# Performance work log

Hardware: AMD Instinct MI355X
Metric: run time of the kernel (lower is better)

## Reference

```python
import jax, jax.numpy as jnp
import numpy as np

NEG_SLOPE = 0.2  # PyG GATConv default negative_slope
N_NODES = 50000


def gat_conv(x, src, dst, W, att_src, att_dst, bias, heads, out_ch):
    # x: [N, F_in]; src/dst: [E] (messages flow src -> dst, softmax over dst)
    N = x.shape[0]
    h = (x @ W).reshape(N, heads, out_ch)              # [N,H,C]
    a_src = jnp.sum(h * att_src, axis=-1)              # [N,H]
    a_dst = jnp.sum(h * att_dst, axis=-1)              # [N,H]
    e = jax.nn.leaky_relu(a_src[src] + a_dst[dst], NEG_SLOPE)   # [E,H]
    # numerically stable segment softmax over incoming edges of each dst node
    m = jax.ops.segment_max(e, dst, num_segments=N)    # [N,H]
    e = jnp.exp(e - m[dst])
    denom = jax.ops.segment_sum(e, dst, num_segments=N)
    alpha = e / (denom[dst] + 1e-16)                   # [E,H]
    msg = h[src] * alpha[:, :, None]                   # [E,H,C]
    out = jax.ops.segment_sum(msg, dst, num_segments=N)  # [N,H,C]
    return out.reshape(N, heads * out_ch) + bias


def add_self_loops(edge_index, num_nodes):
    loop = jnp.arange(num_nodes, dtype=edge_index.dtype)
    return jnp.concatenate([edge_index, jnp.stack([loop, loop])], axis=1)


def setup_inputs() -> dict:
    key = jax.random.key(0)
    ks = jax.random.split(key, 10)
    F_in, H, C, F_out = 256, 4, 64, 16
    x = jax.random.normal(ks[0], (N_NODES, F_in), dtype=jnp.float32)
    edge_index = jax.random.randint(ks[1], (2, 800000), 0, N_NODES, dtype=jnp.int64)
    s1 = 1.0 / np.sqrt(F_in)
    s2 = 1.0 / np.sqrt(H * C)
    return {
        "x": x,
        "edge_index": edge_index,
        "W1": jax.random.normal(ks[2], (F_in, H * C), dtype=jnp.float32) * s1,
        "att_src1": jax.random.normal(ks[3], (H, C), dtype=jnp.float32) * s2,
        "att_dst1": jax.random.normal(ks[4], (H, C), dtype=jnp.float32) * s2,
        "b1": jnp.zeros((H * C,), dtype=jnp.float32),
        "W2": jax.random.normal(ks[5], (H * C, F_out), dtype=jnp.float32) * s2,
        "att_src2": jax.random.normal(ks[6], (1, F_out), dtype=jnp.float32) * 0.25,
        "att_dst2": jax.random.normal(ks[7], (1, F_out), dtype=jnp.float32) * 0.25,
        "b2": jnp.zeros((F_out,), dtype=jnp.float32),
    }


def reference(x, edge_index, W1, att_src1, att_dst1, b1, W2, att_src2, att_dst2, b2):
    ei = add_self_loops(edge_index, x.shape[0])
    src, dst = ei[0], ei[1]
    H1, C1 = att_src1.shape
    h = gat_conv(x, src, dst, W1, att_src1, att_dst1, b1, H1, C1)
    h = jax.nn.relu(h)
    # F.dropout(training=False) is identity in eval mode
    H2, C2 = att_src2.shape
    out = gat_conv(h, src, dst, W2, att_src2, att_dst2, b2, H2, C2)
    return jax.nn.log_softmax(out, axis=1)
```

## Files before the change

### kernel.cpp

```cpp
#include <hip/hip_runtime.h>
#include <math.h>


typedef __attribute__((ext_vector_type(8))) short bf16x8;
typedef __attribute__((ext_vector_type(8))) unsigned short u16x8;
typedef __attribute__((ext_vector_type(4))) float f32x4;
typedef __attribute__((ext_vector_type(2))) float f32x2;

#define BCAP 1536

static __device__ inline unsigned short f2bf(float f) {
    unsigned u = __builtin_bit_cast(unsigned, f);
    unsigned r = (u + 0x7FFF + ((u >> 16) & 1)) >> 16;
    return (unsigned short)r;
}
static __device__ inline float bf2f(unsigned short u) {
    unsigned v = ((unsigned)u) << 16;
    return __builtin_bit_cast(float, v);
}
static __device__ inline float lrelu(float x) { return x > 0.f ? x : 0.2f * x; }

__global__ __launch_bounds__(256) void k_prep(const float* __restrict__ x,
                                              const float* __restrict__ W1,
                                              const float* __restrict__ b1,
                                              const float* __restrict__ W2,
                                              short* __restrict__ xb,
                                              unsigned short* __restrict__ csr,
                                              short* __restrict__ w1t,
                                              float* __restrict__ b1p,
                                              float* __restrict__ w2p,
                                              int* __restrict__ fill_bkt,
                                              float* __restrict__ a1s,
                                              float* __restrict__ a2s,
                                              unsigned* __restrict__ h1f8u,
                                              float* __restrict__ h2,
                                              int N, int nbuk) {
    long idx = (long)blockIdx.x * 256 + threadIdx.x;
    const long T = (long)N * 32;
    if (idx < T) {
        const float* xp = x + idx * 8;
        float4 f0 = *(const float4*)xp;
        float4 f1 = *(const float4*)(xp + 4);
        short b[8];
        b[0] = (short)f2bf(f0.x); b[1] = (short)f2bf(f0.y);
        b[2] = (short)f2bf(f0.z); b[3] = (short)f2bf(f0.w);
        b[4] = (short)f2bf(f1.x); b[5] = (short)f2bf(f1.y);
        b[6] = (short)f2bf(f1.z); b[7] = (short)f2bf(f1.w);
        *(bf16x8*)(xb + idx * 8) = *(bf16x8*)&b[0];
    }
    if (idx < (long)N * 16) {
        ushort4 v = make_ushort4((unsigned short)N, (unsigned short)N,
                                 (unsigned short)N, (unsigned short)N);
        if ((idx & 15) == 0) v.x = (unsigned short)(idx >> 4);
        *(ushort4*)(csr + idx * 4) = v;
    }
    if (idx < nbuk) fill_bkt[idx] = 0;
    if (idx < 256) {
        int ct = ((int)idx >> 6) * 64 + ((int)idx & 3) * 16 + (((int)idx & 63) >> 2);
        b1p[idx] = b1[ct];
    }
    if (idx < 4096) {
        int pp = (int)idx >> 4, c2 = (int)idx & 15;
        int ct = (pp >> 6) * 64 + (pp & 3) * 16 + ((pp & 63) >> 2);
        w2p[idx] = W2[ct * 16 + c2];
    }
    if (idx < 4) a1s[(long)N * 4 + idx] = -1e30f;
    if (idx == 4) a2s[N] = -1e30f;
    if (idx < 64) h1f8u[(long)N * 64 + idx] = 0u;
    if (idx < 16) h2[(long)N * 16 + idx] = 0.f;
    if (idx < 65536) {
        int n = (int)idx >> 8, k = (int)idx & 255;
        w1t[n * 256 + k] = (short)f2bf(W1[k * 256 + n]);
    }
}

__global__ __launch_bounds__(256) void k_bucketize(const int* __restrict__ ei,
                                                   int* __restrict__ fill_bkt,
                                                   unsigned* __restrict__ tmp,
                                                   int E0, int nbuk) {
    __shared__ int hist[1024];
    __shared__ int base[1024];
    const int t = threadIdx.x;
    const int e0 = blockIdx.x * 4096;
    for (int b = t; b < nbuk; b += 256) hist[b] = 0;
    __syncthreads();
    int ss[16], ds[16];
    int nm = 0;
#pragma unroll
    for (int k = 0; k < 16; ++k) {
        int e = e0 + t + k * 256;
        if (e < E0) {
            ss[nm] = ei[e];
            ds[nm] = ei[E0 + e];
            atomicAdd(&hist[ds[nm] >> 6], 1);
            ++nm;
        }
    }
    __syncthreads();
    for (int b = t; b < nbuk; b += 256) {
        int c = hist[b];
        base[b] = c ? atomicAdd(&fill_bkt[b], c) : 0;
        hist[b] = 0;
    }
    __syncthreads();
    for (int k = 0; k < nm; ++k) {
        int b = ds[k] >> 6;
        int r = base[b] + atomicAdd(&hist[b], 1);
        if (r < BCAP)
            tmp[(long)b * BCAP + r] = (unsigned)ss[k] | ((unsigned)(ds[k] & 63) << 16);
    }
}

__global__ __launch_bounds__(256) void k_gemm1_fill(
        const short* __restrict__ Ab,
        const short* __restrict__ Bt,
        const float* __restrict__ att_s,
        const float* __restrict__ att_d,
        unsigned char* __restrict__ C8,
        float* __restrict__ a1s,
        float* __restrict__ a1d,
        int M,
        const unsigned* __restrict__ tmp,
        const int* __restrict__ fill_bkt,
        int* __restrict__ cnt,
        unsigned short* __restrict__ csr,
        int N, int nbuk) {
    __shared__ short As[64][40];
    __shared__ short Bs[128][40];
    __shared__ int lfill[64];

    if ((int)blockIdx.x < nbuk) {
        const int b = blockIdx.x;
        const int t = threadIdx.x;
        if (t < 64) lfill[t] = 0;
        __syncthreads();
        int c = min(fill_bkt[b], BCAP);
        const unsigned* tp = tmp + (long)b * BCAP;
        for (int i = t; i < c; i += 256) {
            unsigned u = tp[i];
            int dl = u >> 16;
            int slot = atomicAdd(&lfill[dl], 1);
            if (slot < 63)
                csr[(((long)b * 64 + dl) << 6) + 1 + slot] = (unsigned short)(u & 0xffff);
        }
        __syncthreads();
        if (t < 64) {
            int d = b * 64 + t;
            if (d < N) cnt[d] = 1 + min(lfill[t], 63);
        }
        return;
    }

    const int g = (int)blockIdx.x - nbuk;
    const int bm = (g >> 1) * 64;
    const int bn = (g & 1) * 128;
    const int tid = threadIdx.x;
    const int lane = tid & 63;
    const int wave = tid >> 6;
    const int wm = (wave >> 1) * 32;
    const int wn = (wave & 1) * 64;
    const int l15 = lane & 15;
    const int l4 = lane >> 4;

    const int ar = tid >> 2, aq = (tid & 3) * 8;
    const int br = tid >> 1, bh = (tid & 1) * 16;

    f32x4 acc[2][4] = {};

    for (int k0 = 0; k0 < 256; k0 += 32) {
        {
            bf16x8 av;
            if (bm + ar < M) {
                av = *(const bf16x8*)&Ab[(long)(bm + ar) * 256 + k0 + aq];
            } else {
#pragma unroll
                for (int q = 0; q < 8; ++q) av[q] = 0;
            }
            *(bf16x8*)&As[ar][aq] = av;
            const short* p = &Bt[(long)(bn + br) * 256 + k0 + bh];
            *(bf16x8*)&Bs[br][bh] = *(const bf16x8*)p;
            *(bf16x8*)&Bs[br][bh + 8] = *(const bf16x8*)(p + 8);
        }
        __syncthreads();

        bf16x8 af[2], bfr[4];
#pragma unroll
        for (int i = 0; i < 2; ++i)
            af[i] = *(const bf16x8*)&As[wm + i * 16 + l15][l4 * 8];
#pragma unroll
        for (int j = 0; j < 4; ++j)
            bfr[j] = *(const bf16x8*)&Bs[wn + j * 16 + l15][l4 * 8];
#pragma unroll
        for (int i = 0; i < 2; ++i)
#pragma unroll
            for (int j = 0; j < 4; ++j)
                acc[i][j] = __builtin_amdgcn_mfma_f32_16x16x32_bf16(af[i], bfr[j], acc[i][j], 0, 0, 0);
        __syncthreads();
    }

    const int h = (bn + wn) >> 6;
    float aws[4], awd[4];
#pragma unroll
    for (int j = 0; j < 4; ++j) {
        aws[j] = att_s[h * 64 + j * 16 + l15];
        awd[j] = att_d[h * 64 + j * 16 + l15];
    }

#pragma unroll
    for (int i = 0; i < 2; ++i) {
#pragma unroll
        for (int r = 0; r < 4; ++r) {
            float sv = 0.f, dv = 0.f;
#pragma unroll
            for (int j = 0; j < 4; ++j) {
                sv += acc[i][j][r] * aws[j];
                dv += acc[i][j][r] * awd[j];
            }
#pragma unroll
            for (int o = 1; o < 16; o <<= 1) {
                sv += __shfl_xor(sv, o);
                dv += __shfl_xor(dv, o);
            }
            int row = bm + wm + i * 16 + l4 * 4 + r;
            if (row < M) {
                if (l15 == 0) { a1s[row * 4 + h] = sv; a1d[row * 4 + h] = dv; }
                int d = 0;
                d = __builtin_amdgcn_cvt_pk_fp8_f32(acc[i][0][r], acc[i][1][r], d, false);
                d = __builtin_amdgcn_cvt_pk_fp8_f32(acc[i][2][r], acc[i][3][r], d, true);
                *(unsigned*)&C8[(long)row * 256 + (bn + wn) + l15 * 4] = (unsigned)d;
            }
        }
    }
}

__global__ __launch_bounds__(256) void k_gather1(const unsigned char* __restrict__ h1f8,
                                                 const int* __restrict__ cnt,
                                                 const unsigned short* __restrict__ csr,
                                                 const float* __restrict__ as1,
                                                 const float* __restrict__ ad1,
                                                 const float* __restrict__ b1p,
                                                 unsigned short* __restrict__ out1b,
                                                 int N) {
    int wid = blockIdx.x * 4 + (threadIdx.x >> 6);
    int lane = threadIdx.x & 63;
    if (wid >= N) return;

    const int es = lane >> 4;
    const int cl = lane & 15;
    const int hc = cl >> 2;
    const float adh = ad1[wid * 4 + hc];

    int c = min(cnt[wid], 64);
    int len4 = (c + 3) & ~3;
    const unsigned short* seg = csr + ((long)wid << 6);
    const char* as1c = (const char*)as1 + hc * 4;
    const char* h1c  = (const char*)h1f8 + cl * 16;

    float dacc = 0.f;
    f32x2 acc2[8] = {};
#pragma unroll 2
    for (int j0 = 0; j0 < len4; j0 += 4) {
        int sv = seg[j0 + es];
        float a = __expf(lrelu(*(const float*)(as1c + ((long)sv << 4)) + adh));
        dacc += a;
        f32x2 av = {a, a};
        uint4 v = *(const uint4*)(h1c + ((long)sv << 8));
        unsigned w[4] = {v.x, v.y, v.z, v.w};
#pragma unroll
        for (int q = 0; q < 4; ++q) {
            f32x2 lo = __builtin_amdgcn_cvt_pk_f32_fp8((int)w[q], false);
            f32x2 hi = __builtin_amdgcn_cvt_pk_f32_fp8((int)w[q], true);
            acc2[q * 2 + 0] += av * lo;
            acc2[q * 2 + 1] += av * hi;
        }
    }
    dacc += __shfl_xor(dacc, 16);
    dacc += __shfl_xor(dacc, 32);
    const float inv_c = 1.f / (dacc + 1e-16f);

    float accf[16];
#pragma unroll
    for (int q = 0; q < 8; ++q) { accf[2 * q] = acc2[q].x; accf[2 * q + 1] = acc2[q].y; }
#pragma unroll
    for (int q = 0; q < 16; ++q) {
        accf[q] += __shfl_xor(accf[q], 16);
        accf[q] += __shfl_xor(accf[q], 32);
    }
    if (lane < 16) {
        unsigned pk[8];
#pragma unroll
        for (int q = 0; q < 8; ++q) {
            float v0 = fmaxf(accf[q * 2 + 0] * inv_c + b1p[cl * 16 + q * 2 + 0], 0.f);
            float v1 = fmaxf(accf[q * 2 + 1] * inv_c + b1p[cl * 16 + q * 2 + 1], 0.f);
            pk[q] = (unsigned)f2bf(v0) | ((unsigned)f2bf(v1) << 16);
        }
        unsigned short* dst = &out1b[(long)wid * 256 + cl * 16];
        *(uint4*)dst = make_uint4(pk[0], pk[1], pk[2], pk[3]);
        *(uint4*)(dst + 8) = make_uint4(pk[4], pk[5], pk[6], pk[7]);
    }
}

__global__ __launch_bounds__(256) void k_gemm2(const unsigned short* __restrict__ Xb,
                                               const float* __restrict__ Wp,
                                               const float* __restrict__ att_s,
                                               const float* __restrict__ att_d,
                                               float* __restrict__ h2,
                                               float* __restrict__ a2s,
                                               float* __restrict__ a2d, int N) {
    __shared__ float Ws[256 * 16];
    for (int i = threadIdx.x; i < 1024; i += 256)
        ((float4*)Ws)[i] = ((const float4*)Wp)[i];
    __syncthreads();
    int r = threadIdx.x >> 4, c = threadIdx.x & 15;
    int row = blockIdx.x * 16 + r;
    if (row >= N) return;
    const unsigned short* xr = Xb + (long)row * 256;
    float acc = 0.f;
    for (int k = 0; k < 256; k += 8) {
        u16x8 xv = *(const u16x8*)&xr[k];
#pragma unroll
        for (int q = 0; q < 8; ++q)
            acc += bf2f(xv[q]) * Ws[(k + q) * 16 + c];
    }
    h2[row * 16 + c] = acc;
    float vs = acc * att_s[c];
    float vd = acc * att_d[c];
    for (int o = 1; o < 16; o <<= 1) { vs += __shfl_xor(vs, o); vd += __shfl_xor(vd, o); }
    if (c == 0) { a2s[row] = vs; a2d[row] = vd; }
}

__global__ __launch_bounds__(256) void k_gather2(const float* __restrict__ h2,
                                                 const int* __restrict__ cnt,
                                                 const unsigned short* __restrict__ csr,
                                                 const float* __restrict__ a2s,
                                                 const float* __restrict__ a2d,
                                                 const float* __restrict__ b2,
                                                 float* __restrict__ out, int N) {
    int wid = blockIdx.x * 4 + (threadIdx.x >> 6);
    int lane = threadIdx.x & 63;
    if (wid >= N) return;
    float adh = a2d[wid];
    const int es = lane >> 2;
    const int c4 = (lane & 3) << 2;

    int cc = min(cnt[wid], 64);
    int len16 = (cc + 15) & ~15;
    const unsigned short* seg = csr + ((long)wid << 6);

    float dacc = 0.f;
    float a0 = 0.f, a1 = 0.f, a2 = 0.f, a3 = 0.f;
    for (int j0 = 0; j0 < len16; j0 += 16) {
        int sv = seg[j0 + es];
        float a = __expf(lrelu(a2s[sv] + adh));
        dacc += a;
        float4 hv = *(const float4*)&h2[((long)sv << 4) + c4];
        a0 += a * hv.x; a1 += a * hv.y; a2 += a * hv.z; a3 += a * hv.w;
    }
#pragma unroll
    for (int o = 4; o < 64; o <<= 1) {
        a0 += __shfl_xor(a0, o); a1 += __shfl_xor(a1, o);
        a2 += __shfl_xor(a2, o); a3 += __shfl_xor(a3, o);
        dacc += __shfl_xor(dacc, o);
    }
    float inv = 1.f / (dacc + 1e-16f);
    float v0 = a0 * inv + b2[c4 + 0];
    float v1 = a1 * inv + b2[c4 + 1];
    float v2 = a2 * inv + b2[c4 + 2];
    float v3 = a3 * inv + b2[c4 + 3];
    float mx = fmaxf(fmaxf(v0, v1), fmaxf(v2, v3));
    mx = fmaxf(mx, __shfl_xor(mx, 1));
    mx = fmaxf(mx, __shfl_xor(mx, 2));
    float se = __expf(v0 - mx) + __expf(v1 - mx) + __expf(v2 - mx) + __expf(v3 - mx);
    se += __shfl_xor(se, 1);
    se += __shfl_xor(se, 2);
    float ls = mx + logf(se);
    if (lane < 4)
        *(float4*)&out[(long)wid * 16 + c4] = make_float4(v0 - ls, v1 - ls, v2 - ls, v3 - ls);
}

extern "C" void kernel_launch(void* const* d_in, const int* in_sizes, int n_in,
                              void* d_out, int out_size, void* d_ws, size_t ws_size,
                              hipStream_t stream) {
    const float* x    = (const float*)d_in[0];
    const int*   ei   = (const int*)d_in[1];
    const float* W1   = (const float*)d_in[2];
    const float* as1w = (const float*)d_in[3];
    const float* ad1w = (const float*)d_in[4];
    const float* b1   = (const float*)d_in[5];
    const float* W2   = (const float*)d_in[6];
    const float* as2w = (const float*)d_in[7];
    const float* ad2w = (const float*)d_in[8];
    const float* b2   = (const float*)d_in[9];
    float* out = (float*)d_out;

    const int N    = in_sizes[0] / 256;
    const int E0   = in_sizes[1] / 2;
    const int NBUK = (N + 63) >> 6;

    char* p = (char*)d_ws;
    unsigned char*  h1f8  = (unsigned char*)p;  p += (size_t)(N + 1) * 256;
    unsigned short* out1b = (unsigned short*)p; p += (size_t)N * 256 * sizeof(short);
    float* h2     = (float*)p; p += (size_t)(N + 1) * 16 * sizeof(float);
    float* a1s    = (float*)p; p += (size_t)(N + 1) * 4 * sizeof(float);
    float* a1d    = (float*)p; p += (size_t)N * 4 * sizeof(float);
    float* a2s    = (float*)p; p += (size_t)(N + 1) * sizeof(float);
    float* a2d    = (float*)p; p += (size_t)N * sizeof(float);
    float* b1p    = (float*)p; p += (size_t)256 * sizeof(float);
    float* w2p    = (float*)p; p += (size_t)4096 * sizeof(float);
    int*   cnt    = (int*)p;   p += (size_t)N * sizeof(int);
    int*   fillbk = (int*)p;   p += (size_t)NBUK * sizeof(int);
    short* w1t    = (short*)p; p += (size_t)256 * 256 * sizeof(short);
    unsigned short* csr = (unsigned short*)p; p += (size_t)N * 64 * sizeof(unsigned short);
    unsigned* tmp = (unsigned*)p; p += (size_t)NBUK * BCAP * sizeof(unsigned);

    short* xb = (short*)out1b;

    const int NW = (N + 3) / 4;

    const long T = (long)N * 32;
    hipLaunchKernelGGL(k_prep, dim3((unsigned)((T + 255) / 256)), dim3(256), 0, stream,
                       x, W1, b1, W2, xb, csr, w1t, b1p, w2p, fillbk, a1s, a2s,
                       (unsigned*)h1f8, h2, N, NBUK);

    hipLaunchKernelGGL(k_bucketize, dim3((E0 + 4095) / 4096), dim3(256), 0, stream,
                       ei, fillbk, tmp, E0, NBUK);

    const int GB = 2 * ((N + 63) / 64);
    hipLaunchKernelGGL(k_gemm1_fill, dim3(NBUK + GB), dim3(256), 0, stream,
                       xb, w1t, as1w, ad1w, h1f8, a1s, a1d, N,
                       tmp, fillbk, cnt, csr, N, NBUK);

    hipLaunchKernelGGL(k_gather1, dim3(NW), dim3(256), 0, stream,
                       h1f8, cnt, csr, a1s, a1d, b1p, out1b, N);

    hipLaunchKernelGGL(k_gemm2, dim3((N + 15) / 16), dim3(256), 0, stream,
                       out1b, w2p, as2w, ad2w, h2, a2s, a2d, N);
    hipLaunchKernelGGL(k_gather2, dim3(NW), dim3(256), 0, stream,
                       h2, cnt, csr, a2s, a2d, b2, out, N);
}
```

Before: 229.4 us.

## Fuse layer-1 gather with layer-2 linear projection and attention scores

Merges the first-layer aggregation kernel with the second-layer GEMM. Each wave keeps its node's 256 post-ReLU features in shared memory and multiplies them by W2, which is staged in LDS per block, to produce h2 and the attention scalars directly. This removes the bf16 intermediate write and re-read plus one kernel launch. In exchange every block reloads the 16KB W2 into LDS, adds a block barrier, and no longer rounds the intermediate to bf16.

```diff
diff --git a/kernel.cpp b/kernel.cpp
--- a/kernel.cpp
+++ b/kernel.cpp
@@ -233,100 +233,110 @@
     }
 }
 
-__global__ __launch_bounds__(256) void k_gather1(const unsigned char* __restrict__ h1f8,
-                                                 const int* __restrict__ cnt,
-                                                 const unsigned short* __restrict__ csr,
-                                                 const float* __restrict__ as1,
-                                                 const float* __restrict__ ad1,
-                                                 const float* __restrict__ b1p,
-                                                 unsigned short* __restrict__ out1b,
-                                                 int N) {
-    int wid = blockIdx.x * 4 + (threadIdx.x >> 6);
-    int lane = threadIdx.x & 63;
-    if (wid >= N) return;
+__global__ __launch_bounds__(256) void k_gather1f(const unsigned char* __restrict__ h1f8,
+                                                  const int* __restrict__ cnt,
+                                                  const unsigned short* __restrict__ csr,
+                                                  const float* __restrict__ as1,
+                                                  const float* __restrict__ ad1,
+                                                  const float* __restrict__ b1p,
+                                                  const float* __restrict__ w2p,
+                                                  const float* __restrict__ as2w,
+                                                  const float* __restrict__ ad2w,
+                                                  float* __restrict__ h2,
+                                                  float* __restrict__ a2s,
+                                                  float* __restrict__ a2d,
+                                                  int N) {
+    __shared__ float Ws[4096];
+    __shared__ float vals[4][256];
+    const int tid = threadIdx.x;
+    for (int i = tid; i < 1024; i += 256)
+        ((float4*)Ws)[i] = ((const float4*)w2p)[i];
+
+    const int wv = tid >> 6;
+    const int lane = tid & 63;
+    const int wid = blockIdx.x * 4 + wv;
+    const bool active = wid < N;
 
     const int es = lane >> 4;
     const int cl = lane & 15;
     const int hc = cl >> 2;
-    const float adh = ad1[wid * 4 + hc];
-
-    int c = min(cnt[wid], 64);
-    int len4 = (c + 3) & ~3;
-    const unsigned short* seg = csr + ((long)wid << 6);
-    const char* as1c = (const char*)as1 + hc * 4;
-    const char* h1c  = (const char*)h1f8 + cl * 16;
-
-    float dacc = 0.f;
-    f32x2 acc2[8] = {};
+
+    float accf[16];
+    float inv_c = 0.f;
+    if (active) {
+        const float adh = ad1[wid * 4 + hc];
+        int c = min(cnt[wid], 64);
+        int len4 = (c + 3) & ~3;
+        const unsigned short* seg = csr + ((long)wid << 6);
+        const char* as1c = (const char*)as1 + hc * 4;
+        const char* h1c  = (const char*)h1f8 + cl * 16;
+
+        float dacc = 0.f;
+        f32x2 acc2[8] = {};
 #pragma unroll 2
-    for (int j0 = 0; j0 < len4; j0 += 4) {
-        int sv = seg[j0 + es];
-        float a = __expf(lrelu(*(const float*)(as1c + ((long)sv << 4)) + adh));
-        dacc += a;
-        f32x2 av = {a, a};
-        uint4 v = *(const uint4*)(h1c + ((long)sv << 8));
-        unsigned w[4] = {v.x, v.y, v.z, v.w};
-#pragma unroll
-        for (int q = 0; q < 4; ++q) {
-            f32x2 lo = __builtin_amdgcn_cvt_pk_f32_fp8((int)w[q], false);
-            f32x2 hi = __builtin_amdgcn_cvt_pk_f32_fp8((int)w[q], true);
-            acc2[q * 2 + 0] += av * lo;
-            acc2[q * 2 + 1] += av * hi;
-        }
-    }
-    dacc += __shfl_xor(dacc, 16);
-    dacc += __shfl_xor(dacc, 32);
-    const float inv_c = 1.f / (dacc + 1e-16f);
-
-    float accf[16];
-#pragma unroll
-    for (int q = 0; q < 8; ++q) { accf[2 * q] = acc2[q].x; accf[2 * q + 1] = acc2[q].y; }
-#pragma unroll
-    for (int q = 0; q < 16; ++q) {
-        accf[q] += __shfl_xor(accf[q], 16);
-        accf[q] += __shfl_xor(accf[q], 32);
-    }
-    if (lane < 16) {
-        unsigned pk[8];
-#pragma unroll
-        for (int q = 0; q < 8; ++q) {
-            float v0 = fmaxf(accf[q * 2 + 0] * inv_c + b1p[cl * 16 + q * 2 + 0], 0.f);
-            float v1 = fmaxf(accf[q * 2 + 1] * inv_c + b1p[cl * 16 + q * 2 + 1], 0.f);
-            pk[q] = (unsigned)f2bf(v0) | ((unsigned)f2bf(v1) << 16);
-        }
-        unsigned short* dst = &out1b[(long)wid * 256 + cl * 16];
-        *(uint4*)dst = make_uint4(pk[0], pk[1], pk[2], pk[3]);
-        *(uint4*)(dst + 8) = make_uint4(pk[4], pk[5], pk[6], pk[7]);
-    }
-}
-
-__global__ __launch_bounds__(256) void k_gemm2(const unsigned short* __restrict__ Xb,
-                                               const float* __restrict__ Wp,
-                                               const float* __restrict__ att_s,
-                                               const float* __restrict__ att_d,
-                                               float* __restrict__ h2,
-                                               float* __restrict__ a2s,
-                                               float* __restrict__ a2d, int N) {
-    __shared__ float Ws[256 * 16];
-    for (int i = threadIdx.x; i < 1024; i += 256)
-        ((float4*)Ws)[i] = ((const float4*)Wp)[i];
+        for (int j0 = 0; j0 < len4; j0 += 4) {
+            int sv = seg[j0 + es];
+            float a = __expf(lrelu(*(const float*)(as1c + ((long)sv << 4)) + adh));
+            dacc += a;
+            f32x2 av = {a, a};
+            uint4 v = *(const uint4*)(h1c + ((long)sv << 8));
+            unsigned w[4] = {v.x, v.y, v.z, v.w};
+#pragma unroll
+            for (int q = 0; q < 4; ++q) {
+                f32x2 lo = __builtin_amdgcn_cvt_pk_f32_fp8((int)w[q], false);
+                f32x2 hi = __builtin_amdgcn_cvt_pk_f32_fp8((int)w[q], true);
+                acc2[q * 2 + 0] += av * lo;
+                acc2[q * 2 + 1] += av * hi;
+            }
+        }
+        dacc += __shfl_xor(dacc, 16);
+        dacc += __shfl_xor(dacc, 32);
+        inv_c = 1.f / (dacc + 1e-16f);
+#pragma unroll
+        for (int q = 0; q < 8; ++q) { accf[2 * q] = acc2[q].x; accf[2 * q + 1] = acc2[q].y; }
+#pragma unroll
+        for (int q = 0; q < 16; ++q) {
+            accf[q] += __shfl_xor(accf[q], 16);
+            accf[q] += __shfl_xor(accf[q], 32);
+        }
+    }
+    if (active && lane < 16) {
+        const float4* bp = (const float4*)(b1p + cl * 16);
+        float4 b0 = bp[0], b1v = bp[1], b2v = bp[2], b3v = bp[3];
+        float* vp = &vals[wv][cl * 16];
+        *(float4*)(vp + 0) = make_float4(
+            fmaxf(accf[0] * inv_c + b0.x, 0.f), fmaxf(accf[1] * inv_c + b0.y, 0.f),
+            fmaxf(accf[2] * inv_c + b0.z, 0.f), fmaxf(accf[3] * inv_c + b0.w, 0.f));
+        *(float4*)(vp + 4) = make_float4(
+            fmaxf(accf[4] * inv_c + b1v.x, 0.f), fmaxf(accf[5] * inv_c + b1v.y, 0.f),
+            fmaxf(accf[6] * inv_c + b1v.z, 0.f), fmaxf(accf[7] * inv_c + b1v.w, 0.f));
+        *(float4*)(vp + 8) = make_float4(
+            fmaxf(accf[8] * inv_c + b2v.x, 0.f), fmaxf(accf[9] * inv_c + b2v.y, 0.f),
+            fmaxf(accf[10] * inv_c + b2v.z, 0.f), fmaxf(accf[11] * inv_c + b2v.w, 0.f));
+        *(float4*)(vp + 12) = make_float4(
+            fmaxf(accf[12] * inv_c + b3v.x, 0.f), fmaxf(accf[13] * inv_c + b3v.y, 0.f),
+            fmaxf(accf[14] * inv_c + b3v.z, 0.f), fmaxf(accf[15] * inv_c + b3v.w, 0.f));
+    }
     __syncthreads();
-    int r = threadIdx.x >> 4, c = threadIdx.x & 15;
-    int row = blockIdx.x * 16 + r;
-    if (row >= N) return;
-    const unsigned short* xr = Xb + (long)row * 256;
-    float acc = 0.f;
-    for (int k = 0; k < 256; k += 8) {
-        u16x8 xv = *(const u16x8*)&xr[k];
-#pragma unroll
-        for (int q = 0; q < 8; ++q)
-            acc += bf2f(xv[q]) * Ws[(k + q) * 16 + c];
-    }
-    h2[row * 16 + c] = acc;
-    float vs = acc * att_s[c];
-    float vd = acc * att_d[c];
-    for (int o = 1; o < 16; o <<= 1) { vs += __shfl_xor(vs, o); vd += __shfl_xor(vd, o); }
-    if (c == 0) { a2s[row] = vs; a2d[row] = vd; }
+
+    if (active) {
+        const int es4 = lane >> 4;
+        float hc_ = 0.f;
+        const float* vp = vals[wv];
+#pragma unroll
+        for (int i = 0; i < 64; ++i) {
+            int k = es4 * 64 + ((i + es4) & 63);
+            hc_ = fmaf(vp[k], Ws[k * 16 + cl], hc_);
+        }
+        hc_ += __shfl_xor(hc_, 16);
+        hc_ += __shfl_xor(hc_, 32);
+        float vs = hc_ * as2w[cl];
+        float vd = hc_ * ad2w[cl];
+#pragma unroll
+        for (int o = 1; o < 16; o <<= 1) { vs += __shfl_xor(vs, o); vd += __shfl_xor(vd, o); }
+        if (lane == 0) { a2s[wid] = vs; a2d[wid] = vd; }
+        if (lane < 16) h2[(long)wid * 16 + cl] = hc_;
+    }
 }
 
 __global__ __launch_bounds__(256) void k_gather2(const float* __restrict__ h2,
@@ -399,7 +409,7 @@
 
     char* p = (char*)d_ws;
     unsigned char*  h1f8  = (unsigned char*)p;  p += (size_t)(N + 1) * 256;
-    unsigned short* out1b = (unsigned short*)p; p += (size_t)N * 256 * sizeof(short);
+    short* xb     = (short*)p; p += (size_t)N * 256 * sizeof(short);
     float* h2     = (float*)p; p += (size_t)(N + 1) * 16 * sizeof(float);
     float* a1s    = (float*)p; p += (size_t)(N + 1) * 4 * sizeof(float);
     float* a1d    = (float*)p; p += (size_t)N * 4 * sizeof(float);
@@ -413,8 +423,6 @@
     unsigned short* csr = (unsigned short*)p; p += (size_t)N * 64 * sizeof(unsigned short);
     unsigned* tmp = (unsigned*)p; p += (size_t)NBUK * BCAP * sizeof(unsigned);
 
-    short* xb = (short*)out1b;
-
     const int NW = (N + 3) / 4;
 
     const long T = (long)N * 32;
@@ -430,11 +438,10 @@
                        xb, w1t, as1w, ad1w, h1f8, a1s, a1d, N,
                        tmp, fillbk, cnt, csr, N, NBUK);
 
-    hipLaunchKernelGGL(k_gather1, dim3(NW), dim3(256), 0, stream,
-                       h1f8, cnt, csr, a1s, a1d, b1p, out1b, N);
-
-    hipLaunchKernelGGL(k_gemm2, dim3((N + 15) / 16), dim3(256), 0, stream,
-                       out1b, w2p, as2w, ad2w, h2, a2s, a2d, N);
+    hipLaunchKernelGGL(k_gather1f, dim3(NW), dim3(256), 0, stream,
+                       h1f8, cnt, csr, a1s, a1d, b1p, w2p, as2w, ad2w,
+                       h2, a2s, a2d, N);
+
     hipLaunchKernelGGL(k_gather2, dim3(NW), dim3(256), 0, stream,
                        h2, cnt, csr, a2s, a2d, b2, out, N);
 }
```

After: 235.9 us. 2.9% more time.
